# Optimization experiments

Measured on AMD Instinct MI355X. Metric: run time of the kernel, lower is better.

Reference implementation:

```python
import jax, jax.numpy as jnp
import numpy as np

B, N, C, H = 4, 2048, 768, 8
D = C // H          # head_size = 96
D3 = D // 3         # projected channel dim = 32


def _linear(x, W, b):
    # torch convention: W [out, in]
    return x @ W.T + b


def setup_inputs() -> dict:
    key = jax.random.key(0)
    ks = jax.random.split(key, 11)
    s = 0.02
    return {
        "x":   jax.random.normal(ks[0], (B, N, C), dtype=jnp.float32),
        "Wqk": jax.random.normal(ks[1], (C, C), dtype=jnp.float32) * s,
        "bqk": jax.random.normal(ks[2], (C,), dtype=jnp.float32) * s,
        "Wv":  jax.random.normal(ks[3], (C, C), dtype=jnp.float32) * s,
        "bv":  jax.random.normal(ks[4], (C,), dtype=jnp.float32) * s,
        "Wo":  jax.random.normal(ks[5], (C, C), dtype=jnp.float32) * s,
        "bo":  jax.random.normal(ks[6], (C,), dtype=jnp.float32) * s,
        "We":  jax.random.normal(ks[7], (D3, D), dtype=jnp.float32) * s,
        "be":  jax.random.normal(ks[8], (D3,), dtype=jnp.float32) * s,
        "Wf":  jax.random.normal(ks[9], (D3, D), dtype=jnp.float32) * s,
        "bf":  jax.random.normal(ks[10], (D3,), dtype=jnp.float32) * s,
    }


def reference(x, Wqk, bqk, Wv, bv, Wo, bo, We, be, Wf, bf):
    b, n, c = x.shape
    # q and k come from the SAME qk_linear applied twice -> identical tensors
    qk = _linear(x, Wqk, bqk).reshape(b, n, H, D)   # [B,N,H,D]
    v_ = _linear(x, Wv, bv).reshape(b, n, H, D)     # [B,N,H,D]

    q = k = qk  # [B,N,H,D] (used as bhnd via einsum)

    # Branch 1: standard softmax attention over tokens
    scale = 1.0 / jnp.sqrt(jnp.asarray(D, dtype=x.dtype))
    scores = jnp.einsum('bnhd,bmhd->bhnm', q, k) * scale   # [B,H,N,N]
    attn = jax.nn.softmax(scores, axis=-1)                  # dropout: identity (eval)
    out1 = jnp.einsum('bhnm,bmhd->bnhd', attn, v_).reshape(b, n, C)
    out1 = _linear(out1, Wo, bo)

    # Branch 2: Linformer-style projected channel attention (per token)
    k_proj = _linear(k, We, be)    # [B,N,H,D3]
    v_proj = _linear(v_, Wf, bf)   # [B,N,H,D3]
    # k_proj^T @ q over heads: [B,N,D3,D], softmax over D
    attn_sa = jax.nn.softmax(jnp.einsum('bnhe,bnhd->bned', k_proj, q), axis=-1)
    x_ca = jnp.einsum('bnhe,bned->bnhd', v_proj, attn_sa).reshape(b, n, C)
    x_ca = _linear(x_ca, Wo, bo)

    return 0.5 * (out1 + x_ca)
```

## Files before the change

kernel.cpp:

```cpp
#include <hip/hip_runtime.h>
#include <math.h>

#define BSZ 4
#define NTOK 2048
#define CDIM 768
#define HN 8
#define DH 96
#define DP 32
#define MTOT (BSZ * NTOK)

typedef short bf16x8 __attribute__((ext_vector_type(8)));
typedef float f32x4 __attribute__((ext_vector_type(4)));

__device__ __forceinline__ unsigned short f2bf(float f) {
    union { float f; unsigned u; } v; v.f = f;
    unsigned r = v.u + 0x7FFFu + ((v.u >> 16) & 1u);
    return (unsigned short)(r >> 16);
}
__device__ __forceinline__ unsigned short f2bf_trunc(float f) {
    union { float f; unsigned u; } v; v.f = f;
    return (unsigned short)(v.u >> 16);
}
__device__ __forceinline__ float bf2f(unsigned short h) {
    union { unsigned u; float f; } v; v.u = ((unsigned)h) << 16;
    return v.f;
}

__device__ __forceinline__ void async16(const unsigned short* g, unsigned short* l) {
    __builtin_amdgcn_global_load_lds(
        (const __attribute__((address_space(1))) unsigned int*)g,
        (__attribute__((address_space(3))) unsigned int*)l,
        16, 0, 0);
}

#define TE4 1572864
#define WE4 147456
#define WE24 768

__global__ __launch_bounds__(256) void prep(const float* __restrict__ x,
                                            const float* __restrict__ Wqk,
                                            const float* __restrict__ Wv,
                                            const float* __restrict__ Wo,
                                            const float* __restrict__ We,
                                            const float* __restrict__ Wf,
                                            unsigned short* __restrict__ xhi,
                                            unsigned short* __restrict__ xlo,
                                            unsigned short* __restrict__ wqv,
                                            unsigned short* __restrict__ woh,
                                            unsigned short* __restrict__ webf,
                                            unsigned short* __restrict__ wfbf)
{
    int i = blockIdx.x * 256 + threadIdx.x;
    if (i < TE4) {
        float4 f = ((const float4*)x)[i];
        ushort4 h, l;
        h.x = f2bf(f.x); l.x = f2bf(f.x - bf2f(h.x));
        h.y = f2bf(f.y); l.y = f2bf(f.y - bf2f(h.y));
        h.z = f2bf(f.z); l.z = f2bf(f.z - bf2f(h.z));
        h.w = f2bf(f.w); l.w = f2bf(f.w - bf2f(h.w));
        ((ushort4*)xhi)[i] = h;
        ((ushort4*)xlo)[i] = l;
        return;
    }
    const float* src; unsigned short* dst; int j;
    if (i < TE4 + WE4)              { j = i - TE4;             src = Wqk; dst = wqv; }
    else if (i < TE4 + 2 * WE4)     { j = i - TE4 - WE4;       src = Wv;  dst = wqv + (size_t)CDIM * CDIM; }
    else if (i < TE4 + 3 * WE4)     { j = i - TE4 - 2 * WE4;   src = Wo;  dst = woh; }
    else if (i < TE4 + 3 * WE4 + WE24) { j = i - TE4 - 3 * WE4; src = We; dst = webf; }
    else                            { j = i - TE4 - 3 * WE4 - WE24; src = Wf; dst = wfbf; }
    float4 f = ((const float4*)src)[j];
    ushort4 u;
    u.x = f2bf(f.x); u.y = f2bf(f.y); u.z = f2bf(f.z); u.w = f2bf(f.w);
    ((ushort4*)dst)[j] = u;
}

#define GSTR 40

__global__ __launch_bounds__(256) void gemm_qv(const unsigned short* __restrict__ Ah,
                                               const unsigned short* __restrict__ Al,
                                               const unsigned short* __restrict__ wqv,
                                               const float* __restrict__ bqk,
                                               const float* __restrict__ bv,
                                               unsigned short* __restrict__ qkbf,
                                               unsigned short* __restrict__ vbf,
                                               unsigned short* __restrict__ vbft)
{
    const int K = CDIM;
    __shared__ __align__(16) unsigned short Ahs[128 * GSTR];
    __shared__ __align__(16) unsigned short Als[128 * GSTR];
    __shared__ __align__(16) unsigned short Bhs[64 * GSTR];

    const int tid  = threadIdx.x;
    const int lane = tid & 63;
    const int w    = tid >> 6;
    const int wy   = w >> 1;
    const int wx   = w & 1;
    const int l15  = lane & 15;
    const int quad = lane >> 4;
    const int n0   = blockIdx.x * 64;
    const int m0   = blockIdx.y * 128;

    f32x4 acc[4][2];
    #pragma unroll
    for (int rb = 0; rb < 4; ++rb)
        #pragma unroll
        for (int cb = 0; cb < 2; ++cb) acc[rb][cb] = (f32x4)0.0f;

    for (int k0 = 0; k0 < K; k0 += 32) {
        #pragma unroll
        for (int p = 0; p < 4; ++p) {
            int idx = tid + p * 256;
            int r = idx >> 3, c4 = idx & 7;
            size_t g = (size_t)(m0 + r) * K + k0 + c4 * 4;
            *(ushort4*)&Ahs[r * GSTR + c4 * 4] = *(const ushort4*)&Ah[g];
            *(ushort4*)&Als[r * GSTR + c4 * 4] = *(const ushort4*)&Al[g];
        }
        #pragma unroll
        for (int p = 0; p < 2; ++p) {
            int idx = tid + p * 256;
            int r = idx >> 3, c4 = idx & 7;
            size_t g = (size_t)(n0 + r) * K + k0 + c4 * 4;
            *(ushort4*)&Bhs[r * GSTR + c4 * 4] = *(const ushort4*)&wqv[g];
        }
        __syncthreads();

        bf16x8 ah[4], al[4], bh[2];
        #pragma unroll
        for (int rb = 0; rb < 4; ++rb) {
            int off = (wy * 64 + rb * 16 + l15) * GSTR + quad * 8;
            ah[rb] = *(const bf16x8*)&Ahs[off];
            al[rb] = *(const bf16x8*)&Als[off];
        }
        #pragma unroll
        for (int cb = 0; cb < 2; ++cb)
            bh[cb] = *(const bf16x8*)&Bhs[(wx * 32 + cb * 16 + l15) * GSTR + quad * 8];

        #pragma unroll
        for (int rb = 0; rb < 4; ++rb)
            #pragma unroll
            for (int cb = 0; cb < 2; ++cb) {
                acc[rb][cb] = __builtin_amdgcn_mfma_f32_16x16x32_bf16(ah[rb], bh[cb], acc[rb][cb], 0, 0, 0);
                acc[rb][cb] = __builtin_amdgcn_mfma_f32_16x16x32_bf16(al[rb], bh[cb], acc[rb][cb], 0, 0, 0);
            }
        __syncthreads();
    }

    const bool isQ = (n0 < CDIM);
    #pragma unroll
    for (int rb = 0; rb < 4; ++rb)
        #pragma unroll
        for (int cb = 0; cb < 2; ++cb)
            #pragma unroll
            for (int r = 0; r < 4; ++r) {
                int row = m0 + wy * 64 + rb * 16 + quad * 4 + r;
                int colg = n0 + wx * 32 + cb * 16 + l15;
                if (isQ) {
                    float val = acc[rb][cb][r] + bqk[colg];
                    qkbf[(size_t)row * CDIM + colg] = f2bf(val);
                } else {
                    int col = colg - CDIM;
                    float val = acc[rb][cb][r] + bv[col];
                    vbf[(size_t)row * CDIM + col] = f2bf(val);
                    int b = row >> 11, tok = row & 2047;
                    int hh = col / DH, dd = col % DH;
                    vbft[(((size_t)b * HN + hh) * DH + dd) * NTOK + tok] = f2bf(val);
                }
            }
}

#define PSTR 104

__global__ __launch_bounds__(256) void proj_gemm(const unsigned short* __restrict__ qkbf,
                                                 const unsigned short* __restrict__ vbf,
                                                 const unsigned short* __restrict__ webf,
                                                 const unsigned short* __restrict__ wfbf,
                                                 const float* __restrict__ be,
                                                 const float* __restrict__ bfv,
                                                 float* __restrict__ kp,
                                                 float* __restrict__ vp)
{
    const unsigned short* Abf = blockIdx.y ? vbf : qkbf;
    const unsigned short* Wbf = blockIdx.y ? wfbf : webf;
    const float* bias         = blockIdx.y ? bfv : be;
    float* Y                  = blockIdx.y ? vp : kp;

    __shared__ __align__(16) unsigned short As[128 * PSTR];
    __shared__ __align__(16) unsigned short Bs[32 * PSTR];

    const int tid  = threadIdx.x;
    const int lane = tid & 63;
    const int w    = tid >> 6;
    const int l15  = lane & 15;
    const int quad = lane >> 4;
    const int m0   = blockIdx.x * 128;

    {
        int r = tid & 127;
        int cb = (tid >> 7) * 12;
        #pragma unroll
        for (int t = 0; t < 12; ++t) {
            int c4 = cb + t;
            if (c4 < 24)
                *(ushort4*)&As[r * PSTR + c4 * 4] =
                    *(const ushort4*)&Abf[(size_t)(m0 + r) * DH + c4 * 4];
        }
    }
    #pragma unroll
    for (int t = 0; t < 3; ++t) {
        int idx = tid + t * 256;
        if (idx < 32 * 24) {
            int r = idx / 24, c4 = idx % 24;
            *(ushort4*)&Bs[r * PSTR + c4 * 4] = *(const ushort4*)&Wbf[r * DH + c4 * 4];
        }
    }
    __syncthreads();

    f32x4 acc[2][2];
    #pragma unroll
    for (int rb = 0; rb < 2; ++rb)
        #pragma unroll
        for (int cb = 0; cb < 2; ++cb) acc[rb][cb] = (f32x4)0.0f;

    #pragma unroll
    for (int kf = 0; kf < 3; ++kf) {
        bf16x8 a0 = *(const bf16x8*)&As[(w * 32 + l15) * PSTR + kf * 32 + quad * 8];
        bf16x8 a1 = *(const bf16x8*)&As[(w * 32 + 16 + l15) * PSTR + kf * 32 + quad * 8];
        bf16x8 b0 = *(const bf16x8*)&Bs[(l15) * PSTR + kf * 32 + quad * 8];
        bf16x8 b1 = *(const bf16x8*)&Bs[(16 + l15) * PSTR + kf * 32 + quad * 8];
        acc[0][0] = __builtin_amdgcn_mfma_f32_16x16x32_bf16(a0, b0, acc[0][0], 0, 0, 0);
        acc[0][1] = __builtin_amdgcn_mfma_f32_16x16x32_bf16(a0, b1, acc[0][1], 0, 0, 0);
        acc[1][0] = __builtin_amdgcn_mfma_f32_16x16x32_bf16(a1, b0, acc[1][0], 0, 0, 0);
        acc[1][1] = __builtin_amdgcn_mfma_f32_16x16x32_bf16(a1, b1, acc[1][1], 0, 0, 0);
    }

    #pragma unroll
    for (int rb = 0; rb < 2; ++rb)
        #pragma unroll
        for (int cb = 0; cb < 2; ++cb)
            #pragma unroll
            for (int r = 0; r < 4; ++r) {
                int row = m0 + w * 32 + rb * 16 + quad * 4 + r;
                int col = cb * 16 + l15;
                Y[(size_t)row * DP + col] = acc[rb][cb][r] + bias[col];
            }
}

#define QT 128
#define KT 32
#define PST 40
#define SCL2 0.14724420f

__global__ __launch_bounds__(256) void attn_mfma(const unsigned short* __restrict__ qk_bf,
                                                 const unsigned short* __restrict__ v_bft,
                                                 unsigned short* __restrict__ chi)
{
    __shared__ __align__(16) unsigned short KfS[2][6 * 512];
    __shared__ __align__(16) unsigned short VfS[2][6 * 512];
    __shared__ __align__(16) unsigned short Ps[QT * PST];

    const int tid  = threadIdx.x;
    const int lane = tid & 63;
    const int w    = tid >> 6;
    const int l15  = lane & 15;
    const int quad = lane >> 4;

    const int bid = blockIdx.x;
    const int bh  = (bid & 7) * 4 + ((bid >> 3) & 3);
    const int qt  = bid >> 5;
    const int b   = bh >> 3;
    const int h   = bh & 7;
    const int q0  = qt * QT;

    const unsigned short* qbase = qk_bf + (size_t)b * NTOK * CDIM + h * DH;
    const unsigned short* vtb   = v_bft + (size_t)(b * HN + h) * DH * NTOK;

    bf16x8 qf[2][3];
    #pragma unroll
    for (int rb = 0; rb < 2; ++rb)
        #pragma unroll
        for (int kf = 0; kf < 3; ++kf)
            qf[rb][kf] = *(const bf16x8*)&qbase[(size_t)(q0 + w * 32 + rb * 16 + l15) * CDIM + kf * 32 + quad * 8];

    const int  kjt   = w;
    const int  vd0   = (w - 2) * 3;
    const unsigned short* kgb = qbase + (size_t)(kjt * 16 + l15) * CDIM + quad * 8;
    const unsigned short* vgb = vtb + quad * 8;

    bf16x8 ones;
    #pragma unroll
    for (int i = 0; i < 8; ++i) ones[i] = (short)0x3F80;

    f32x4 o[2][6], ls[2];
    #pragma unroll
    for (int rb = 0; rb < 2; ++rb) {
        ls[rb] = (f32x4)0.0f;
        #pragma unroll
        for (int db = 0; db < 6; ++db) o[rb][db] = (f32x4)0.0f;
    }

    if (w < 2) {
        #pragma unroll
        for (int kf = 0; kf < 3; ++kf)
            async16(kgb + kf * 32, &KfS[0][(kf * 2 + kjt) * 512]);
    } else {
        #pragma unroll
        for (int t = 0; t < 3; ++t)
            async16(vgb + (size_t)((vd0 + t) * 16 + l15) * NTOK, &VfS[0][(vd0 + t) * 512]);
    }
    __syncthreads();

    int cur = 0;
    for (int k0 = 0; k0 < NTOK; k0 += KT) {
        const int nxt = cur ^ 1;
        if (k0 + KT < NTOK) {
            if (w < 2) {
                #pragma unroll
                for (int kf = 0; kf < 3; ++kf)
                    async16(kgb + (size_t)(k0 + KT) * CDIM + kf * 32, &KfS[nxt][(kf * 2 + kjt) * 512]);
            } else {
                #pragma unroll
                for (int t = 0; t < 3; ++t)
                    async16(vgb + (size_t)((vd0 + t) * 16 + l15) * NTOK + k0 + KT, &VfS[nxt][(vd0 + t) * 512]);
            }
        }

        f32x4 s00 = (f32x4)0.0f, s01 = (f32x4)0.0f, s10 = (f32x4)0.0f, s11 = (f32x4)0.0f;
        #pragma unroll
        for (int kf = 0; kf < 3; ++kf) {
            bf16x8 k0f = *(const bf16x8*)&KfS[cur][(kf * 2 + 0) * 512 + lane * 8];
            bf16x8 k1f = *(const bf16x8*)&KfS[cur][(kf * 2 + 1) * 512 + lane * 8];
            s00 = __builtin_amdgcn_mfma_f32_16x16x32_bf16(qf[0][kf], k0f, s00, 0, 0, 0);
            s01 = __builtin_amdgcn_mfma_f32_16x16x32_bf16(qf[0][kf], k1f, s01, 0, 0, 0);
            s10 = __builtin_amdgcn_mfma_f32_16x16x32_bf16(qf[1][kf], k0f, s10, 0, 0, 0);
            s11 = __builtin_amdgcn_mfma_f32_16x16x32_bf16(qf[1][kf], k1f, s11, 0, 0, 0);
        }

        #pragma unroll
        for (int r = 0; r < 4; ++r) {
            int pr0 = w * 32 + quad * 4 + r;
            Ps[pr0 * PST + l15]      = f2bf_trunc(exp2f(s00[r] * SCL2));
            Ps[pr0 * PST + l15 + 16] = f2bf_trunc(exp2f(s01[r] * SCL2));
            int pr1 = pr0 + 16;
            Ps[pr1 * PST + l15]      = f2bf_trunc(exp2f(s10[r] * SCL2));
            Ps[pr1 * PST + l15 + 16] = f2bf_trunc(exp2f(s11[r] * SCL2));
        }

        bf16x8 pf0 = *(const bf16x8*)&Ps[(w * 32 + l15) * PST + quad * 8];
        bf16x8 pf1 = *(const bf16x8*)&Ps[(w * 32 + 16 + l15) * PST + quad * 8];
        ls[0] = __builtin_amdgcn_mfma_f32_16x16x32_bf16(pf0, ones, ls[0], 0, 0, 0);
        ls[1] = __builtin_amdgcn_mfma_f32_16x16x32_bf16(pf1, ones, ls[1], 0, 0, 0);
        #pragma unroll
        for (int db = 0; db < 6; ++db) {
            bf16x8 vf = *(const bf16x8*)&VfS[cur][db * 512 + lane * 8];
            o[0][db] = __builtin_amdgcn_mfma_f32_16x16x32_bf16(pf0, vf, o[0][db], 0, 0, 0);
            o[1][db] = __builtin_amdgcn_mfma_f32_16x16x32_bf16(pf1, vf, o[1][db], 0, 0, 0);
        }

        __syncthreads();
        cur = nxt;
    }

    #pragma unroll
    for (int rb = 0; rb < 2; ++rb)
        #pragma unroll
        for (int r = 0; r < 4; ++r) {
            float inv = 1.0f / ls[rb][r];
            int row = w * 32 + rb * 16 + quad * 4 + r;
            size_t base = ((size_t)b * NTOK + q0 + row) * CDIM + h * DH;
            #pragma unroll
            for (int db = 0; db < 6; ++db)
                chi[base + db * 16 + l15] = f2bf(o[rb][db][r] * inv);
        }
}

#define SFS 97

__global__ __launch_bounds__(256) void branch2_v2(const unsigned short* __restrict__ qkbf,
                                                  const float* __restrict__ kpG,
                                                  const float* __restrict__ vpG,
                                                  unsigned short* __restrict__ chi)
{
    __shared__ float qrowS[CDIM];
    __shared__ float SfS[DP * SFS];
    __shared__ float kpS[HN * DP];
    __shared__ float vpS[HN * DP];
    __shared__ float ps[DP][8];
    __shared__ float invs[DP];

    const int tid = threadIdx.x;
    const size_t tok = blockIdx.x;

    if (tid < 192) {
        ushort4 u = *(const ushort4*)&qkbf[tok * CDIM + tid * 4];
        float4 f;
        f.x = bf2f(u.x); f.y = bf2f(u.y); f.z = bf2f(u.z); f.w = bf2f(u.w);
        *(float4*)&qrowS[tid * 4] = f;
    } else {
        int t = tid - 192;
        ((float4*)kpS)[t] = ((const float4*)(kpG + tok * (HN * DP)))[t];
        ((float4*)vpS)[t] = ((const float4*)(vpG + tok * (HN * DP)))[t];
    }
    __syncthreads();

    #pragma unroll
    for (int t = 0; t < 12; ++t) {
        int idx = tid + t * 256;
        int e = idx / DH, d = idx % DH;
        float s = 0.0f;
        #pragma unroll
        for (int h = 0; h < HN; ++h) s += kpS[h * DP + e] * qrowS[h * DH + d];
        SfS[e * SFS + d] = exp2f(s * 1.44269504f);
    }
    __syncthreads();

    {
        int e = tid >> 3, g = tid & 7;
        float s = 0.0f;
        #pragma unroll
        for (int j = 0; j < 12; ++j) s += SfS[e * SFS + g * 12 + j];
        ps[e][g] = s;
    }
    __syncthreads();
    if (tid < DP) {
        float s = 0.0f;
        #pragma unroll
        for (int g = 0; g < 8; ++g) s += ps[tid][g];
        invs[tid] = 1.0f / s;
    }
    __syncthreads();
    {
        int h = tid >> 5, e = tid & 31;
        vpS[h * DP + e] *= invs[e];
    }
    __syncthreads();

    #pragma unroll
    for (int t = 0; t < 3; ++t) {
        int c = tid + t * 256;
        int h = c / DH, d = c % DH;
        float s = 0.0f;
        #pragma unroll 8
        for (int e = 0; e < DP; ++e) s += vpS[h * DP + e] * SfS[e * SFS + d];
        size_t idx = tok * CDIM + c;
        chi[idx] = f2bf(bf2f(chi[idx]) + s);
    }
}

__global__ __launch_bounds__(256) void gemm_out(const unsigned short* __restrict__ Ah,
                                                const unsigned short* __restrict__ Bh,
                                                const float* __restrict__ bias,
                                                float* __restrict__ Yf)
{
    const int N = CDIM, K = CDIM;
    __shared__ __align__(16) unsigned short Ahs[128 * GSTR];
    __shared__ __align__(16) unsigned short Bhs[64 * GSTR];

    const int tid  = threadIdx.x;
    const int lane = tid & 63;
    const int w    = tid >> 6;
    const int wy   = w >> 1;
    const int wx   = w & 1;
    const int l15  = lane & 15;
    const int quad = lane >> 4;
    const int n0   = blockIdx.x * 64;
    const int m0   = blockIdx.y * 128;

    f32x4 acc[4][2];
    #pragma unroll
    for (int rb = 0; rb < 4; ++rb)
        #pragma unroll
        for (int cb = 0; cb < 2; ++cb) acc[rb][cb] = (f32x4)0.0f;

    for (int k0 = 0; k0 < K; k0 += 32) {
        #pragma unroll
        for (int p = 0; p < 4; ++p) {
            int idx = tid + p * 256;
            int r = idx >> 3, c4 = idx & 7;
            *(ushort4*)&Ahs[r * GSTR + c4 * 4] =
                *(const ushort4*)&Ah[(size_t)(m0 + r) * K + k0 + c4 * 4];
        }
        #pragma unroll
        for (int p = 0; p < 2; ++p) {
            int idx = tid + p * 256;
            int r = idx >> 3, c4 = idx & 7;
            *(ushort4*)&Bhs[r * GSTR + c4 * 4] =
                *(const ushort4*)&Bh[(size_t)(n0 + r) * K + k0 + c4 * 4];
        }
        __syncthreads();

        bf16x8 ah[4], bh[2];
        #pragma unroll
        for (int rb = 0; rb < 4; ++rb)
            ah[rb] = *(const bf16x8*)&Ahs[(wy * 64 + rb * 16 + l15) * GSTR + quad * 8];
        #pragma unroll
        for (int cb = 0; cb < 2; ++cb)
            bh[cb] = *(const bf16x8*)&Bhs[(wx * 32 + cb * 16 + l15) * GSTR + quad * 8];

        #pragma unroll
        for (int rb = 0; rb < 4; ++rb)
            #pragma unroll
            for (int cb = 0; cb < 2; ++cb)
                acc[rb][cb] = __builtin_amdgcn_mfma_f32_16x16x32_bf16(ah[rb], bh[cb], acc[rb][cb], 0, 0, 0);
        __syncthreads();
    }

    #pragma unroll
    for (int rb = 0; rb < 4; ++rb)
        #pragma unroll
        for (int cb = 0; cb < 2; ++cb)
            #pragma unroll
            for (int r = 0; r < 4; ++r) {
                int row = m0 + wy * 64 + rb * 16 + quad * 4 + r;
                int col = n0 + wx * 32 + cb * 16 + l15;
                Yf[(size_t)row * N + col] = 0.5f * acc[rb][cb][r] + bias[col];
            }
}

extern "C" void kernel_launch(void* const* d_in, const int* in_sizes, int n_in,
                              void* d_out, int out_size, void* d_ws, size_t ws_size,
                              hipStream_t stream)
{
    (void)in_sizes; (void)n_in; (void)out_size; (void)ws_size;
    const float* x   = (const float*)d_in[0];
    const float* Wqk = (const float*)d_in[1];
    const float* bqk = (const float*)d_in[2];
    const float* Wv  = (const float*)d_in[3];
    const float* bv  = (const float*)d_in[4];
    const float* Wo  = (const float*)d_in[5];
    const float* bo  = (const float*)d_in[6];
    const float* We  = (const float*)d_in[7];
    const float* be  = (const float*)d_in[8];
    const float* Wf  = (const float*)d_in[9];
    const float* bfv = (const float*)d_in[10];
    float* out = (float*)d_out;

    const size_t TE  = (size_t)MTOT * CDIM;
    const size_t WE  = (size_t)CDIM * CDIM;
    const size_t WE2 = (size_t)DP * DH;
    const size_t PE  = (size_t)MTOT * HN * DP;

    char* p = (char*)d_ws;
    unsigned short* xhi  = (unsigned short*)p;   p += TE * 2;
    unsigned short* xlo  = (unsigned short*)p;   p += TE * 2;
    unsigned short* qkbf = (unsigned short*)p;   p += TE * 2;
    unsigned short* vbf  = (unsigned short*)p;   p += TE * 2;
    unsigned short* vbft = (unsigned short*)p;   p += TE * 2;
    unsigned short* chi  = (unsigned short*)p;   p += TE * 2;
    unsigned short* wqv  = (unsigned short*)p;   p += 2 * WE * 2;
    unsigned short* woh  = (unsigned short*)p;   p += WE * 2;
    unsigned short* webf = (unsigned short*)p;   p += WE2 * 2;
    unsigned short* wfbf = (unsigned short*)p;   p += WE2 * 2;
    float* kp            = (float*)p;            p += PE * 4;
    float* vp            = (float*)p;            p += PE * 4;

    const int prep_items = TE4 + 3 * WE4 + 2 * WE24;
    prep<<<dim3((prep_items + 255) / 256), 256, 0, stream>>>(
        x, Wqk, Wv, Wo, We, Wf, xhi, xlo, wqv, woh, webf, wfbf);

    gemm_qv<<<dim3(2 * CDIM / 64, MTOT / 128), 256, 0, stream>>>(
        xhi, xlo, wqv, bqk, bv, qkbf, vbf, vbft);

    proj_gemm<<<dim3(MTOT * HN / 128, 2), 256, 0, stream>>>(
        qkbf, vbf, webf, wfbf, be, bfv, kp, vp);

    attn_mfma<<<dim3((NTOK / QT) * BSZ * HN), 256, 0, stream>>>(qkbf, vbft, chi);

    branch2_v2<<<dim3(MTOT), 256, 0, stream>>>(qkbf, kp, vp, chi);

    gemm_out<<<dim3(CDIM / 64, MTOT / 128), 256, 0, stream>>>(chi, woh, bo, out);
}
```

Measured before the change: 344.2 us.

## Drop x lo-split and double-buffer GEMM tiles with async global-to-LDS loads

Stops splitting x into bf16 hi and lo parts, so the QV projection runs one MFMA per tile instead of two and skips writing and reading the lo buffer. Both the QV and output GEMMs now stage A and B tiles through global_load_lds async copies into a double-buffered, fragment-ordered LDS layout. The next k-tile is prefetched while the current one is multiplied, and one barrier per iteration replaces two. Dropping the lo term lowers the precision of the QK and V projections, which risks tolerance failures.

```diff
diff --git a/kernel.cpp b/kernel.cpp
--- a/kernel.cpp
+++ b/kernel.cpp
@@ -44,40 +44,26 @@
                                             const float* __restrict__ We,
                                             const float* __restrict__ Wf,
                                             unsigned short* __restrict__ xhi,
-                                            unsigned short* __restrict__ xlo,
                                             unsigned short* __restrict__ wqv,
                                             unsigned short* __restrict__ woh,
                                             unsigned short* __restrict__ webf,
                                             unsigned short* __restrict__ wfbf)
 {
     int i = blockIdx.x * 256 + threadIdx.x;
-    if (i < TE4) {
-        float4 f = ((const float4*)x)[i];
-        ushort4 h, l;
-        h.x = f2bf(f.x); l.x = f2bf(f.x - bf2f(h.x));
-        h.y = f2bf(f.y); l.y = f2bf(f.y - bf2f(h.y));
-        h.z = f2bf(f.z); l.z = f2bf(f.z - bf2f(h.z));
-        h.w = f2bf(f.w); l.w = f2bf(f.w - bf2f(h.w));
-        ((ushort4*)xhi)[i] = h;
-        ((ushort4*)xlo)[i] = l;
-        return;
-    }
     const float* src; unsigned short* dst; int j;
-    if (i < TE4 + WE4)              { j = i - TE4;             src = Wqk; dst = wqv; }
-    else if (i < TE4 + 2 * WE4)     { j = i - TE4 - WE4;       src = Wv;  dst = wqv + (size_t)CDIM * CDIM; }
-    else if (i < TE4 + 3 * WE4)     { j = i - TE4 - 2 * WE4;   src = Wo;  dst = woh; }
-    else if (i < TE4 + 3 * WE4 + WE24) { j = i - TE4 - 3 * WE4; src = We; dst = webf; }
-    else                            { j = i - TE4 - 3 * WE4 - WE24; src = Wf; dst = wfbf; }
+    if (i < TE4)                        { j = i;                        src = x;   dst = xhi; }
+    else if (i < TE4 + WE4)             { j = i - TE4;                  src = Wqk; dst = wqv; }
+    else if (i < TE4 + 2 * WE4)         { j = i - TE4 - WE4;            src = Wv;  dst = wqv + (size_t)CDIM * CDIM; }
+    else if (i < TE4 + 3 * WE4)         { j = i - TE4 - 2 * WE4;        src = Wo;  dst = woh; }
+    else if (i < TE4 + 3 * WE4 + WE24)  { j = i - TE4 - 3 * WE4;        src = We;  dst = webf; }
+    else                                { j = i - TE4 - 3 * WE4 - WE24; src = Wf;  dst = wfbf; }
     float4 f = ((const float4*)src)[j];
     ushort4 u;
     u.x = f2bf(f.x); u.y = f2bf(f.y); u.z = f2bf(f.z); u.w = f2bf(f.w);
     ((ushort4*)dst)[j] = u;
 }
 
-#define GSTR 40
-
 __global__ __launch_bounds__(256) void gemm_qv(const unsigned short* __restrict__ Ah,
-                                               const unsigned short* __restrict__ Al,
                                                const unsigned short* __restrict__ wqv,
                                                const float* __restrict__ bqk,
                                                const float* __restrict__ bv,
@@ -86,9 +72,7 @@
                                                unsigned short* __restrict__ vbft)
 {
     const int K = CDIM;
-    __shared__ __align__(16) unsigned short Ahs[128 * GSTR];
-    __shared__ __align__(16) unsigned short Als[128 * GSTR];
-    __shared__ __align__(16) unsigned short Bhs[64 * GSTR];
+    __shared__ __align__(16) unsigned short S[2][12 * 512];
 
     const int tid  = threadIdx.x;
     const int lane = tid & 63;
@@ -100,49 +84,51 @@
     const int n0   = blockIdx.x * 64;
     const int m0   = blockIdx.y * 128;
 
+    const unsigned short* gsrc[3];
+    #pragma unroll
+    for (int t = 0; t < 3; ++t) {
+        int c = 3 * w + t;
+        gsrc[t] = (c < 8)
+            ? Ah  + (size_t)(m0 + c * 16 + l15) * K + quad * 8
+            : wqv + (size_t)(n0 + (c - 8) * 16 + l15) * K + quad * 8;
+    }
+
     f32x4 acc[4][2];
     #pragma unroll
     for (int rb = 0; rb < 4; ++rb)
         #pragma unroll
         for (int cb = 0; cb < 2; ++cb) acc[rb][cb] = (f32x4)0.0f;
 
+    #pragma unroll
+    for (int t = 0; t < 3; ++t)
+        async16(gsrc[t], &S[0][(3 * w + t) * 512]);
+    __syncthreads();
+
+    int cur = 0;
     for (int k0 = 0; k0 < K; k0 += 32) {
-        #pragma unroll
-        for (int p = 0; p < 4; ++p) {
-            int idx = tid + p * 256;
-            int r = idx >> 3, c4 = idx & 7;
-            size_t g = (size_t)(m0 + r) * K + k0 + c4 * 4;
-            *(ushort4*)&Ahs[r * GSTR + c4 * 4] = *(const ushort4*)&Ah[g];
-            *(ushort4*)&Als[r * GSTR + c4 * 4] = *(const ushort4*)&Al[g];
-        }
-        #pragma unroll
-        for (int p = 0; p < 2; ++p) {
-            int idx = tid + p * 256;
-            int r = idx >> 3, c4 = idx & 7;
-            size_t g = (size_t)(n0 + r) * K + k0 + c4 * 4;
-            *(ushort4*)&Bhs[r * GSTR + c4 * 4] = *(const ushort4*)&wqv[g];
-        }
+        const int nxt = cur ^ 1;
+        if (k0 + 32 < K) {
+            #pragma unroll
+            for (int t = 0; t < 3; ++t)
+                async16(gsrc[t] + k0 + 32, &S[nxt][(3 * w + t) * 512]);
+        }
+
+        bf16x8 a[4], bfr[2];
+        #pragma unroll
+        for (int rb = 0; rb < 4; ++rb)
+            a[rb] = *(const bf16x8*)&S[cur][(wy * 4 + rb) * 512 + lane * 8];
+        #pragma unroll
+        for (int cb = 0; cb < 2; ++cb)
+            bfr[cb] = *(const bf16x8*)&S[cur][(8 + wx * 2 + cb) * 512 + lane * 8];
+
+        #pragma unroll
+        for (int rb = 0; rb < 4; ++rb)
+            #pragma unroll
+            for (int cb = 0; cb < 2; ++cb)
+                acc[rb][cb] = __builtin_amdgcn_mfma_f32_16x16x32_bf16(a[rb], bfr[cb], acc[rb][cb], 0, 0, 0);
+
         __syncthreads();
-
-        bf16x8 ah[4], al[4], bh[2];
-        #pragma unroll
-        for (int rb = 0; rb < 4; ++rb) {
-            int off = (wy * 64 + rb * 16 + l15) * GSTR + quad * 8;
-            ah[rb] = *(const bf16x8*)&Ahs[off];
-            al[rb] = *(const bf16x8*)&Als[off];
-        }
-        #pragma unroll
-        for (int cb = 0; cb < 2; ++cb)
-            bh[cb] = *(const bf16x8*)&Bhs[(wx * 32 + cb * 16 + l15) * GSTR + quad * 8];
-
-        #pragma unroll
-        for (int rb = 0; rb < 4; ++rb)
-            #pragma unroll
-            for (int cb = 0; cb < 2; ++cb) {
-                acc[rb][cb] = __builtin_amdgcn_mfma_f32_16x16x32_bf16(ah[rb], bh[cb], acc[rb][cb], 0, 0, 0);
-                acc[rb][cb] = __builtin_amdgcn_mfma_f32_16x16x32_bf16(al[rb], bh[cb], acc[rb][cb], 0, 0, 0);
-            }
-        __syncthreads();
+        cur = nxt;
     }
 
     const bool isQ = (n0 < CDIM);
@@ -452,8 +438,7 @@
                                                 float* __restrict__ Yf)
 {
     const int N = CDIM, K = CDIM;
-    __shared__ __align__(16) unsigned short Ahs[128 * GSTR];
-    __shared__ __align__(16) unsigned short Bhs[64 * GSTR];
+    __shared__ __align__(16) unsigned short S[2][12 * 512];
 
     const int tid  = threadIdx.x;
     const int lane = tid & 63;
@@ -465,43 +450,51 @@
     const int n0   = blockIdx.x * 64;
     const int m0   = blockIdx.y * 128;
 
+    const unsigned short* gsrc[3];
+    #pragma unroll
+    for (int t = 0; t < 3; ++t) {
+        int c = 3 * w + t;
+        gsrc[t] = (c < 8)
+            ? Ah + (size_t)(m0 + c * 16 + l15) * K + quad * 8
+            : Bh + (size_t)(n0 + (c - 8) * 16 + l15) * K + quad * 8;
+    }
+
     f32x4 acc[4][2];
     #pragma unroll
     for (int rb = 0; rb < 4; ++rb)
         #pragma unroll
         for (int cb = 0; cb < 2; ++cb) acc[rb][cb] = (f32x4)0.0f;
 
+    #pragma unroll
+    for (int t = 0; t < 3; ++t)
+        async16(gsrc[t], &S[0][(3 * w + t) * 512]);
+    __syncthreads();
+
+    int cur = 0;
     for (int k0 = 0; k0 < K; k0 += 32) {
-        #pragma unroll
-        for (int p = 0; p < 4; ++p) {
-            int idx = tid + p * 256;
-            int r = idx >> 3, c4 = idx & 7;
-            *(ushort4*)&Ahs[r * GSTR + c4 * 4] =
-                *(const ushort4*)&Ah[(size_t)(m0 + r) * K + k0 + c4 * 4];
-        }
-        #pragma unroll
-        for (int p = 0; p < 2; ++p) {
-            int idx = tid + p * 256;
-            int r = idx >> 3, c4 = idx & 7;
-            *(ushort4*)&Bhs[r * GSTR + c4 * 4] =
-                *(const ushort4*)&Bh[(size_t)(n0 + r) * K + k0 + c4 * 4];
-        }
+        const int nxt = cur ^ 1;
+        if (k0 + 32 < K) {
+            #pragma unroll
+            for (int t = 0; t < 3; ++t)
+                async16(gsrc[t] + k0 + 32, &S[nxt][(3 * w + t) * 512]);
+        }
+
+        bf16x8 a[4], bfr[2];
+        #pragma unroll
+        for (int rb = 0; rb < 4; ++rb)
+            a[rb] = *(const bf16x8*)&S[cur][(wy * 4 + rb) * 512 + lane * 8];
+        #pragma unroll
+        for (int cb = 0; cb < 2; ++cb)
+            bfr[cb] = *(const bf16x8*)&S[cur][(8 + wx * 2 + cb) * 512 + lane * 8];
+
+        #pragma unroll
+        for (int rb = 0; rb < 4; ++rb)
+            #pragma unroll
+            for (int cb = 0; cb < 2; ++cb)
+                acc[rb][cb] = __builtin_amdgcn_mfma_f32_16x16x32_bf16(a[rb], bfr[cb], acc[rb][cb], 0, 0, 0);
+
         __syncthreads();
-
-        bf16x8 ah[4], bh[2];
-        #pragma unroll
-        for (int rb = 0; rb < 4; ++rb)
-            ah[rb] = *(const bf16x8*)&Ahs[(wy * 64 + rb * 16 + l15) * GSTR + quad * 8];
-        #pragma unroll
-        for (int cb = 0; cb < 2; ++cb)
-            bh[cb] = *(const bf16x8*)&Bhs[(wx * 32 + cb * 16 + l15) * GSTR + quad * 8];
-
-        #pragma unroll
-        for (int rb = 0; rb < 4; ++rb)
-            #pragma unroll
-            for (int cb = 0; cb < 2; ++cb)
-                acc[rb][cb] = __builtin_amdgcn_mfma_f32_16x16x32_bf16(ah[rb], bh[cb], acc[rb][cb], 0, 0, 0);
-        __syncthreads();
+        cur = nxt;
     }
 
     #pragma unroll
@@ -541,7 +534,6 @@
 
     char* p = (char*)d_ws;
     unsigned short* xhi  = (unsigned short*)p;   p += TE * 2;
-    unsigned short* xlo  = (unsigned short*)p;   p += TE * 2;
     unsigned short* qkbf = (unsigned short*)p;   p += TE * 2;
     unsigned short* vbf  = (unsigned short*)p;   p += TE * 2;
     unsigned short* vbft = (unsigned short*)p;   p += TE * 2;
@@ -555,10 +547,10 @@
 
     const int prep_items = TE4 + 3 * WE4 + 2 * WE24;
     prep<<<dim3((prep_items + 255) / 256), 256, 0, stream>>>(
-        x, Wqk, Wv, Wo, We, Wf, xhi, xlo, wqv, woh, webf, wfbf);
+        x, Wqk, Wv, Wo, We, Wf, xhi, wqv, woh, webf, wfbf);
 
     gemm_qv<<<dim3(2 * CDIM / 64, MTOT / 128), 256, 0, stream>>>(
-        xhi, xlo, wqv, bqk, bv, qkbf, vbf, vbft);
+        xhi, wqv, bqk, bv, qkbf, vbf, vbft);
 
     proj_gemm<<<dim3(MTOT * HN / 128, 2), 256, 0, stream>>>(
         qkbf, vbf, webf, wfbf, be, bfv, kp, vp);
```

Result: no change. 342.4 us (-0.5%).
